# Optimization experiments

Measured on AMD Instinct MI355X. Metric: run time of the kernel, lower is better.

Reference implementation:

```python
import jax, jax.numpy as jnp
import numpy as np

I4_CLIP = 7.0
NUM_HEADS = 16
NUM_KV_HEADS = 4
HEAD_DIM = 64
ROPE_BASE = 10000.0


def fake_quant_i4(w):
    # per-row int4 symmetric fake quantization with straight-through estimator
    row_max = jnp.maximum(jnp.max(jnp.abs(w), axis=-1, keepdims=True), 1e-8)
    scale = row_max / I4_CLIP
    w_deq = jnp.clip(jnp.round(w / scale), -I4_CLIP, I4_CLIP) * scale
    return w + jax.lax.stop_gradient(w_deq - w)


def rms_norm(x):
    eps = jnp.asarray(jnp.finfo(x.dtype).eps, x.dtype)
    return x * jax.lax.rsqrt(jnp.mean(x * x, axis=-1, keepdims=True) + eps)


def rope_cos_sin(seqlen, dtype):
    inv_freq = 1.0 / (ROPE_BASE ** (jnp.arange(0, HEAD_DIM, 2, dtype=jnp.float32) / HEAD_DIM))
    freqs = jnp.outer(jnp.arange(seqlen, dtype=jnp.float32), inv_freq)  # [S, hd/2]
    return jnp.cos(freqs).astype(dtype), jnp.sin(freqs).astype(dtype)


def apply_rotary(x, cos, sin):
    # x: [B, H, S, hd]; cos/sin: [S, hd/2] broadcast over B, H
    half = x.shape[-1] // 2
    x1, x2 = x[..., :half], x[..., half:]
    return jnp.concatenate((x1 * cos + x2 * sin, -x1 * sin + x2 * cos), axis=-1)


def setup_inputs() -> dict:
    key = jax.random.key(0)
    ks = jax.random.split(key, 6)
    dim = NUM_HEADS * HEAD_DIM
    kv_dim = NUM_KV_HEADS * HEAD_DIM
    return {
        "x": jax.random.normal(ks[0], (2, 2048, dim), jnp.float32),
        "w_q": jax.random.normal(ks[1], (dim, dim), jnp.float32) * 0.02,
        "w_k": jax.random.normal(ks[2], (kv_dim, dim), jnp.float32) * 0.02,
        "w_v": jax.random.normal(ks[3], (kv_dim, dim), jnp.float32) * 0.02,
        "w_proj": jax.random.normal(ks[4], (dim, dim), jnp.float32) * 0.02,
        "q_gain": jnp.ones((NUM_HEADS,), jnp.float32),
    }


def reference(x, w_q, w_k, w_v, w_proj, q_gain):
    bsz, seqlen, dim = x.shape
    rep = NUM_HEADS // NUM_KV_HEADS

    wq, wk, wv, wp = (fake_quant_i4(w) for w in (w_q, w_k, w_v, w_proj))

    # projections: F.linear(x, W) = x @ W.T -> [B, S, out]; split heads -> [B, H, S, hd]
    q = (x @ wq.T).reshape(bsz, seqlen, NUM_HEADS, HEAD_DIM).transpose(0, 2, 1, 3)
    k = (x @ wk.T).reshape(bsz, seqlen, NUM_KV_HEADS, HEAD_DIM).transpose(0, 2, 1, 3)
    v = (x @ wv.T).reshape(bsz, seqlen, NUM_KV_HEADS, HEAD_DIM).transpose(0, 2, 1, 3)

    q, k = rms_norm(q), rms_norm(k)
    cos, sin = rope_cos_sin(seqlen, q.dtype)
    q = apply_rotary(q, cos, sin)
    k = apply_rotary(k, cos, sin)
    q = q * q_gain.astype(q.dtype)[None, :, None, None]

    # GQA: expand kv heads
    k = jnp.repeat(k, rep, axis=1)
    v = jnp.repeat(v, rep, axis=1)

    # causal SDPA
    scale = 1.0 / np.sqrt(HEAD_DIM)
    scores = jnp.einsum("bhqd,bhkd->bhqk", q, k) * scale
    causal = jnp.tril(jnp.ones((seqlen, seqlen), dtype=bool))
    scores = jnp.where(causal, scores, jnp.asarray(-jnp.inf, scores.dtype))
    attn = jax.nn.softmax(scores, axis=-1)
    y = jnp.einsum("bhqk,bhkd->bhqd", attn, v)

    y = y.transpose(0, 2, 1, 3).reshape(bsz, seqlen, dim)
    return y @ wp.T
```

## Files before the change

kernel.cpp:

```cpp
#include <hip/hip_runtime.h>


typedef __bf16 bf16x8 __attribute__((ext_vector_type(8)));
typedef __bf16 bf16x4 __attribute__((ext_vector_type(4)));
typedef float  f32x4  __attribute__((ext_vector_type(4)));

__device__ __forceinline__ unsigned short f2bf(float f) {
  __bf16 h = (__bf16)f;
  return __builtin_bit_cast(unsigned short, h);
}

__global__ void quant_rows(const float* __restrict__ src,
                           unsigned short* __restrict__ dst, int ncols) {
  int row = blockIdx.x;
  const float* s = src + (size_t)row * ncols;
  unsigned short* d = dst + (size_t)row * ncols;
  int t = threadIdx.x;
  float v[4]; float mx = 0.f;
#pragma unroll
  for (int i = 0; i < 4; i++) { v[i] = s[t + 256 * i]; mx = fmaxf(mx, fabsf(v[i])); }
#pragma unroll
  for (int m = 1; m < 64; m <<= 1) mx = fmaxf(mx, __shfl_xor(mx, m));
  __shared__ float smx[4];
  if ((t & 63) == 0) smx[t >> 6] = mx;
  __syncthreads();
  mx = fmaxf(fmaxf(smx[0], smx[1]), fmaxf(smx[2], smx[3]));
  mx = fmaxf(mx, 1e-8f);
  float scale = mx / 7.0f;
#pragma unroll
  for (int i = 0; i < 4; i++) {
    float q = rintf(v[i] / scale);
    q = fminf(fmaxf(q, -7.0f), 7.0f);
    d[t + 256 * i] = f2bf(q * scale);
  }
}

__global__ void cvt_bf16(const float* __restrict__ src,
                         unsigned short* __restrict__ dst, int n) {
  int i = (blockIdx.x * 256 + threadIdx.x) * 4;
  if (i >= n) return;
  float4 f = *(const float4*)(src + i);
  ushort4 o;
  o.x = f2bf(f.x); o.y = f2bf(f.y); o.z = f2bf(f.z); o.w = f2bf(f.w);
  *(ushort4*)(dst + i) = o;
}

#define GLDS(g, l)                                                            \
  __builtin_amdgcn_global_load_lds((const __attribute__((address_space(1))) void*)(g), \
                                   (__attribute__((address_space(3))) void*)(l), 16, 0, 0)

__global__ __launch_bounds__(256, 2) void gemm_bt(
    const unsigned short* __restrict__ A, const unsigned short* __restrict__ Bw,
    float* __restrict__ C, int N, int K, int nbn) {
  int bm = blockIdx.x / nbn, bn = blockIdx.x % nbn;
  int tid = threadIdx.x, w = tid >> 6, lane = tid & 63;
  int l15 = lane & 15, lh = lane >> 4;
  __shared__ __align__(16) unsigned short ldsA[2][128 * 64];
  __shared__ __align__(16) unsigned short ldsB[2][128 * 64];
  int wr = w >> 1, wc = w & 1;
  f32x4 zero = {0.f, 0.f, 0.f, 0.f};
  f32x4 acc[4][4];
#pragma unroll
  for (int i = 0; i < 4; i++)
#pragma unroll
    for (int j = 0; j < 4; j++) acc[i][j] = zero;

  int srow = lane >> 3, schunk = (lane & 7) ^ (lane >> 3);
  const unsigned short* gA0 = A  + (size_t)(bm * 128 + srow) * K + schunk * 8;
  const unsigned short* gB0 = Bw + (size_t)(bn * 128 + srow) * K + schunk * 8;

  int nk = K >> 6;
#pragma unroll
  for (int it = 0; it < 4; it++) {
    int seg = w * 4 + it;
    GLDS(gA0 + (size_t)(seg * 8) * K, (unsigned short*)ldsA[0] + seg * 512);
    GLDS(gB0 + (size_t)(seg * 8) * K, (unsigned short*)ldsB[0] + seg * 512);
  }
  __syncthreads();
  int cur = 0;
  for (int kt = 0; kt < nk; kt++) {
    if (kt + 1 < nk) {
      int k0 = (kt + 1) * 64;
#pragma unroll
      for (int it = 0; it < 4; it++) {
        int seg = w * 4 + it;
        GLDS(gA0 + (size_t)(seg * 8) * K + k0, (unsigned short*)ldsA[cur ^ 1] + seg * 512);
        GLDS(gB0 + (size_t)(seg * 8) * K + k0, (unsigned short*)ldsB[cur ^ 1] + seg * 512);
      }
    }
    const unsigned short* cA = ldsA[cur];
    const unsigned short* cB = ldsB[cur];
#pragma unroll
    for (int ks = 0; ks < 2; ks++) {
      bf16x8 af[4], bfr[4];
#pragma unroll
      for (int fm = 0; fm < 4; fm++) {
        int row = wr * 64 + fm * 16 + l15;
        int slot = (ks * 4 + lh) ^ (row & 7);
        af[fm] = *(const bf16x8*)(cA + row * 64 + slot * 8);
      }
#pragma unroll
      for (int fn = 0; fn < 4; fn++) {
        int row = wc * 64 + fn * 16 + l15;
        int slot = (ks * 4 + lh) ^ (row & 7);
        bfr[fn] = *(const bf16x8*)(cB + row * 64 + slot * 8);
      }
#pragma unroll
      for (int fm = 0; fm < 4; fm++)
#pragma unroll
        for (int fn = 0; fn < 4; fn++)
          acc[fm][fn] = __builtin_amdgcn_mfma_f32_16x16x32_bf16(af[fm], bfr[fn], acc[fm][fn], 0, 0, 0);
    }
    __syncthreads();
    cur ^= 1;
  }
#pragma unroll
  for (int fm = 0; fm < 4; fm++) {
    int r0 = bm * 128 + wr * 64 + fm * 16 + lh * 4;
#pragma unroll
    for (int fn = 0; fn < 4; fn++) {
      int c = bn * 128 + wc * 64 + fn * 16 + l15;
#pragma unroll
      for (int reg = 0; reg < 4; reg++)
        C[(size_t)(r0 + reg) * N + c] = acc[fm][fn][reg];
    }
  }
}

__global__ __launch_bounds__(256, 2) void gemm_qkv(
    const unsigned short* __restrict__ A, const unsigned short* __restrict__ Bw,
    const float* __restrict__ gainp,
    unsigned short* __restrict__ qb, unsigned short* __restrict__ kbp,
    unsigned short* __restrict__ vbp) {
  const int K = 1024;
  int bm = blockIdx.x / 12, bn = blockIdx.x % 12;
  int tid = threadIdx.x, w = tid >> 6, lane = tid & 63;
  int l15 = lane & 15, lh = lane >> 4;
  __shared__ __align__(16) unsigned short ldsA[2][128 * 64];
  __shared__ __align__(16) unsigned short ldsB[2][128 * 64];
  int wr = w >> 1, wc = w & 1;
  f32x4 zero = {0.f, 0.f, 0.f, 0.f};
  f32x4 acc[4][4];
#pragma unroll
  for (int i = 0; i < 4; i++)
#pragma unroll
    for (int j = 0; j < 4; j++) acc[i][j] = zero;

  int srow = lane >> 3, schunk = (lane & 7) ^ (lane >> 3);
  const unsigned short* gA0 = A  + (size_t)(bm * 128 + srow) * K + schunk * 8;
  const unsigned short* gB0 = Bw + (size_t)(bn * 128 + srow) * K + schunk * 8;

#pragma unroll
  for (int it = 0; it < 4; it++) {
    int seg = w * 4 + it;
    GLDS(gA0 + (size_t)(seg * 8) * K, (unsigned short*)ldsA[0] + seg * 512);
    GLDS(gB0 + (size_t)(seg * 8) * K, (unsigned short*)ldsB[0] + seg * 512);
  }
  __syncthreads();
  int cur = 0;
  for (int kt = 0; kt < 16; kt++) {
    if (kt + 1 < 16) {
      int k0 = (kt + 1) * 64;
#pragma unroll
      for (int it = 0; it < 4; it++) {
        int seg = w * 4 + it;
        GLDS(gA0 + (size_t)(seg * 8) * K + k0, (unsigned short*)ldsA[cur ^ 1] + seg * 512);
        GLDS(gB0 + (size_t)(seg * 8) * K + k0, (unsigned short*)ldsB[cur ^ 1] + seg * 512);
      }
    }
    const unsigned short* cA = ldsA[cur];
    const unsigned short* cB = ldsB[cur];
#pragma unroll
    for (int ks = 0; ks < 2; ks++) {
      bf16x8 af[4], bfr[4];
#pragma unroll
      for (int fm = 0; fm < 4; fm++) {
        int row = wr * 64 + fm * 16 + l15;
        int slot = (ks * 4 + lh) ^ (row & 7);
        af[fm] = *(const bf16x8*)(cA + row * 64 + slot * 8);
      }
#pragma unroll
      for (int fn = 0; fn < 4; fn++) {
        int row = wc * 64 + fn * 16 + l15;
        int slot = (ks * 4 + lh) ^ (row & 7);
        bfr[fn] = *(const bf16x8*)(cB + row * 64 + slot * 8);
      }
#pragma unroll
      for (int fm = 0; fm < 4; fm++)
#pragma unroll
        for (int fn = 0; fn < 4; fn++)
          acc[fm][fn] = __builtin_amdgcn_mfma_f32_16x16x32_bf16(af[fm], bfr[fn], acc[fm][fn], 0, 0, 0);
    }
    __syncthreads();
    cur ^= 1;
  }

  int hid = bn * 2 + wc;
  int rbase = bm * 128 + wr * 64;
  if (hid >= 20) {
    int vh = hid - 20;
#pragma unroll
    for (int fm = 0; fm < 4; fm++)
#pragma unroll
      for (int reg = 0; reg < 4; reg++) {
        int r = rbase + fm * 16 + lh * 4 + reg;
        int b = r >> 11, s = r & 2047;
        unsigned short* dst = vbp + (((size_t)(b * 4 + vh) * 2048 + s) << 6);
#pragma unroll
        for (int fn = 0; fn < 4; fn++)
          dst[fn * 16 + l15] = f2bf(acc[fm][fn][reg]);
      }
  } else {
    bool isq = hid < 16;
    float gn = isq ? gainp[hid] : 1.0f;
    float invf0 = __expf(-0.28782313662425572f * (float)l15);
    float invf1 = __expf(-0.28782313662425572f * (float)(l15 + 16));
#pragma unroll
    for (int fm = 0; fm < 4; fm++)
#pragma unroll
      for (int reg = 0; reg < 4; reg++) {
        float y0 = acc[fm][0][reg], y1 = acc[fm][1][reg];
        float y2 = acc[fm][2][reg], y3 = acc[fm][3][reg];
        float ss = y0 * y0 + y1 * y1 + y2 * y2 + y3 * y3;
        ss += __shfl_xor(ss, 1); ss += __shfl_xor(ss, 2);
        ss += __shfl_xor(ss, 4); ss += __shfl_xor(ss, 8);
        float rn = rsqrtf(ss * 0.015625f + 1.1920929e-7f);
        y0 *= rn; y1 *= rn; y2 *= rn; y3 *= rn;
        int r = rbase + fm * 16 + lh * 4 + reg;
        int b = r >> 11, s = r & 2047;
        float c0, s0n, c1, s1n;
        __sincosf((float)s * invf0, &s0n, &c0);
        __sincosf((float)s * invf1, &s1n, &c1);
        float o0 = (y0 * c0 + y2 * s0n) * gn;
        float o1 = (y1 * c1 + y3 * s1n) * gn;
        float o2 = (y2 * c0 - y0 * s0n) * gn;
        float o3 = (y3 * c1 - y1 * s1n) * gn;
        unsigned short* dst = isq
          ? qb  + (((size_t)(b * 16 + hid) * 2048 + s) << 6)
          : kbp + (((size_t)(b * 4 + (hid - 16)) * 2048 + s) << 6);
        dst[l15]      = f2bf(o0);
        dst[l15 + 16] = f2bf(o1);
        dst[l15 + 32] = f2bf(o2);
        dst[l15 + 48] = f2bf(o3);
      }
  }
}

__global__ void v_transpose(const unsigned short* __restrict__ vbp,
                            unsigned short* __restrict__ vt) {
  int bid = blockIdx.x;
  int st = bid & 31, bk = bid >> 5;
  __shared__ unsigned short tile[64][72];
  int t = threadIdx.x;
  int sl = t >> 2, d0 = (t & 3) * 16;
  const unsigned short* src = vbp + (((size_t)bk * 2048 + st * 64 + sl) << 6) + d0;
  *(ushort4*)&tile[sl][d0]      = *(const ushort4*)(src);
  *(ushort4*)&tile[sl][d0 + 4]  = *(const ushort4*)(src + 4);
  *(ushort4*)&tile[sl][d0 + 8]  = *(const ushort4*)(src + 8);
  *(ushort4*)&tile[sl][d0 + 12] = *(const ushort4*)(src + 12);
  __syncthreads();
  int d = t >> 2, p0 = (t & 3) * 16;
  unsigned short* dst = vt + ((size_t)bk * 64 + d) * 2048 + st * 64 + p0;
#pragma unroll
  for (int jo = 0; jo < 16; jo += 4) {
    ushort4 a;
#pragma unroll
    for (int j = 0; j < 4; j++) {
      int p = p0 + jo + j;
      int c = ((p & 3) << 4) | (p >> 2);
      ((unsigned short*)&a)[j] = tile[c][d];
    }
    *(ushort4*)(dst + jo) = a;
  }
}

#define PSTR 72

template<bool MASK>
__device__ __forceinline__ void attn_tile(
    int kv0, int q0, int l15, int lh, float M2,
    const unsigned short* ldsK, const unsigned short* ldsV, unsigned short* pw,
    const bf16x8 (&qf)[2][2], float (&lsum)[2][4], f32x4 (&o)[2][4]) {
  const float K2 = 0.18033688011112042f;
  f32x4 zero = {0.f, 0.f, 0.f, 0.f};
  f32x4 sc[2][4];
#pragma unroll
  for (int fm = 0; fm < 2; fm++)
#pragma unroll
    for (int fn = 0; fn < 4; fn++) sc[fm][fn] = zero;
#pragma unroll
  for (int ks = 0; ks < 2; ks++) {
    bf16x8 kf[4];
#pragma unroll
    for (int fn = 0; fn < 4; fn++) {
      int row = fn * 16 + l15;
      int slot = (ks * 4 + lh) ^ (row & 7);
      kf[fn] = *(const bf16x8*)(ldsK + row * 64 + slot * 8);
    }
#pragma unroll
    for (int fm = 0; fm < 2; fm++)
#pragma unroll
      for (int fn = 0; fn < 4; fn++)
        sc[fm][fn] = __builtin_amdgcn_mfma_f32_16x16x32_bf16(qf[fm][ks], kf[fn], sc[fm][fn], 0, 0, 0);
  }
#pragma unroll
  for (int fm = 0; fm < 2; fm++)
#pragma unroll
    for (int r = 0; r < 4; r++) {
      bf16x4 pk;
      float ls = 0.f;
#pragma unroll
      for (int fn = 0; fn < 4; fn++) {
        float s = __builtin_fmaf(sc[fm][fn][r], K2, -M2);
        if (MASK) {
          int col = kv0 + fn * 16 + l15;
          int row = q0 + fm * 16 + lh * 4 + r;
          if (col > row) s = -1e30f;
        }
        float p = __builtin_amdgcn_exp2f(s);
        ls += p;
        pk[fn] = (__bf16)p;
      }
      *(bf16x4*)(pw + (fm * 16 + lh * 4 + r) * PSTR + l15 * 4) = pk;
      lsum[fm][r] += ls;
    }
  asm volatile("s_waitcnt lgkmcnt(0)" ::: "memory");
  __builtin_amdgcn_sched_barrier(0);
#pragma unroll
  for (int ks2 = 0; ks2 < 2; ks2++) {
    bf16x8 vf[4], pf[2];
#pragma unroll
    for (int fn = 0; fn < 4; fn++) {
      int row = fn * 16 + l15;
      int slot = (ks2 * 4 + lh) ^ (row & 7);
      vf[fn] = *(const bf16x8*)(ldsV + row * 64 + slot * 8);
    }
#pragma unroll
    for (int fm = 0; fm < 2; fm++)
      pf[fm] = *(const bf16x8*)(pw + (fm * 16 + l15) * PSTR + ks2 * 32 + lh * 8);
#pragma unroll
    for (int fm = 0; fm < 2; fm++)
#pragma unroll
      for (int fn = 0; fn < 4; fn++)
        o[fm][fn] = __builtin_amdgcn_mfma_f32_16x16x32_bf16(pf[fm], vf[fn], o[fm][fn], 0, 0, 0);
  }
}

__global__ __launch_bounds__(256, 3) void attn_fwd(
    const unsigned short* __restrict__ qbuf, const unsigned short* __restrict__ kb,
    const unsigned short* __restrict__ vtb, const float* __restrict__ gain,
    unsigned short* __restrict__ ob, float* __restrict__ pO,
    float* __restrict__ pL) {
  int bid = blockIdx.x;
  int cid = 39 - (bid >> 5);
  int bh = bid & 31;
  int b = bh >> 4, h = bh & 15;
  int q, ch;
  if (cid < 4)       { q = cid;             ch = 0; }
  else if (cid < 12) { q = (cid + 4) >> 1;  ch = (cid + 4) & 1; }
  else if (cid < 24) { q = (cid + 12) / 3;  ch = (cid + 12) % 3; }
  else               { q = (cid + 24) >> 2; ch = (cid + 24) & 3; }
  int nt = 2 * q + 2;
  int t0 = ch * 8;
  int t1 = (t0 + 8 < nt) ? t0 + 8 : nt;
  bool direct = (cid < 4);

  int tid = threadIdx.x;
  int w = tid >> 6, lane = tid & 63;
  int l15 = lane & 15, lh = lane >> 4;
  int q0 = q * 128 + w * 32;
  int kvh = h >> 2;
  const unsigned short* Q  = qbuf + (size_t)(b * 16 + h) * (2048 * 64);
  const unsigned short* Kg = kb   + (size_t)(b * 4 + kvh) * (2048 * 64);
  const unsigned short* Vg = vtb  + (size_t)(b * 4 + kvh) * (64 * 2048);

  __shared__ __align__(16) unsigned short ldsK[2][64 * 64];
  __shared__ __align__(16) unsigned short ldsV[2][64 * 64];
  __shared__ __align__(16) unsigned short plds[4][32 * PSTR];
  unsigned short* pw = plds[w];

  float gn = gain[h];
  float M2 = __builtin_fmaf(fabsf(gn), 1.46f, 0.02f);

  bf16x8 qf[2][2];
#pragma unroll
  for (int fm = 0; fm < 2; fm++)
#pragma unroll
    for (int ks = 0; ks < 2; ks++)
      qf[fm][ks] = *(const bf16x8*)(Q + (q0 + fm * 16 + l15) * 64 + ks * 32 + lh * 8);

  f32x4 zero = {0.f, 0.f, 0.f, 0.f};
  f32x4 o[2][4];
  float lsum[2][4];
#pragma unroll
  for (int fm = 0; fm < 2; fm++)
#pragma unroll
    for (int r = 0; r < 4; r++) { lsum[fm][r] = 0.f; o[fm][r] = zero; }

  int srow = lane >> 3;
  int schunk = (lane & 7) ^ (lane >> 3);
  int full = q0 >> 6;

#pragma unroll
  for (int it = 0; it < 2; it++) {
    int seg = w * 2 + it;
    GLDS(Kg + (size_t)(t0 * 64 + seg * 8 + srow) * 64 + schunk * 8,
         (unsigned short*)ldsK[0] + seg * 512);
    GLDS(Vg + (size_t)(seg * 8 + srow) * 2048 + t0 * 64 + schunk * 8,
         (unsigned short*)ldsV[0] + seg * 512);
  }
  __syncthreads();
  int cur = 0;
  for (int t = t0; t < t1; t++) {
    int kv0 = t * 64;
    if (t + 1 < t1) {
      int kn = kv0 + 64;
#pragma unroll
      for (int it = 0; it < 2; it++) {
        int seg = w * 2 + it;
        GLDS(Kg + (size_t)(kn + seg * 8 + srow) * 64 + schunk * 8,
             (unsigned short*)ldsK[cur ^ 1] + seg * 512);
        GLDS(Vg + (size_t)(seg * 8 + srow) * 2048 + kn + schunk * 8,
             (unsigned short*)ldsV[cur ^ 1] + seg * 512);
      }
    }
    if (t < full)
      attn_tile<false>(kv0, q0, l15, lh, M2, ldsK[cur], ldsV[cur], pw, qf, lsum, o);
    else if (kv0 <= q0 + 31)
      attn_tile<true>(kv0, q0, l15, lh, M2, ldsK[cur], ldsV[cur], pw, qf, lsum, o);
    __syncthreads();
    cur ^= 1;
  }

  if (direct) {
#pragma unroll
    for (int fm = 0; fm < 2; fm++)
#pragma unroll
      for (int r = 0; r < 4; r++) {
        float l = lsum[fm][r];
        l += __shfl_xor(l, 1); l += __shfl_xor(l, 2);
        l += __shfl_xor(l, 4); l += __shfl_xor(l, 8);
        float inv = 1.0f / l;
        int row = q0 + fm * 16 + lh * 4 + r;
#pragma unroll
        for (int fn = 0; fn < 4; fn++)
          ob[(size_t)(b * 2048 + row) * 1024 + h * 64 + fn * 16 + l15] =
              f2bf(o[fm][fn][r] * inv);
      }
  } else {
    int slot = bh * 36 + (cid - 4);
    float* po = pO + ((size_t)slot << 13);
    float* pl = pL + slot * 128;
#pragma unroll
    for (int fm = 0; fm < 2; fm++)
#pragma unroll
      for (int r = 0; r < 4; r++) {
        float l = lsum[fm][r];
        l += __shfl_xor(l, 1); l += __shfl_xor(l, 2);
        l += __shfl_xor(l, 4); l += __shfl_xor(l, 8);
        int row = w * 32 + fm * 16 + lh * 4 + r;
        if (l15 == 0) pl[row] = l;
#pragma unroll
        for (int fn = 0; fn < 4; fn++)
          po[row * 64 + fn * 16 + l15] = o[fm][fn][r];
      }
  }
}

__global__ __launch_bounds__(256) void attn_finalize(
    const float* __restrict__ pO, const float* __restrict__ pL,
    unsigned short* __restrict__ ob) {
  int bid = blockIdx.x;
  int q = 4 + (bid % 12);
  int bh = bid / 12;
  int b = bh >> 4, h = bh & 15;
  int nc = (2 * q + 9) >> 3;
  int cum = (q < 8) ? 2 * q - 4 : ((q < 12) ? 3 * q - 12 : 4 * q - 24);
  int sbase = bh * 36 + (cum - 4);

  int tid = threadIdx.x;
  int row = tid >> 1, half = tid & 1;
  f32x4 s[8];
#pragma unroll
  for (int j = 0; j < 8; j++) s[j] = (f32x4){0.f, 0.f, 0.f, 0.f};
  float l = 0.f;
  for (int c = 0; c < nc; c++) {
    const float* po = pO + (((size_t)(sbase + c)) << 13) + row * 64 + half * 32;
    l += pL[(sbase + c) * 128 + row];
#pragma unroll
    for (int j = 0; j < 8; j++) s[j] += *(const f32x4*)(po + j * 4);
  }
  float inv = 1.0f / l;
  unsigned short* dst =
      ob + (size_t)(b * 2048 + q * 128 + row) * 1024 + h * 64 + half * 32;
#pragma unroll
  for (int j = 0; j < 8; j++) {
    ushort4 u;
    u.x = f2bf(s[j][0] * inv); u.y = f2bf(s[j][1] * inv);
    u.z = f2bf(s[j][2] * inv); u.w = f2bf(s[j][3] * inv);
    *(ushort4*)(dst + j * 4) = u;
  }
}

extern "C" void kernel_launch(void* const* d_in, const int* in_sizes, int n_in,
                              void* d_out, int out_size, void* d_ws, size_t ws_size,
                              hipStream_t stream) {
  const float* x    = (const float*)d_in[0];
  const float* w_q  = (const float*)d_in[1];
  const float* w_k  = (const float*)d_in[2];
  const float* w_v  = (const float*)d_in[3];
  const float* w_p  = (const float*)d_in[4];
  const float* gain = (const float*)d_in[5];
  float* out = (float*)d_out;

  char* ws = (char*)d_ws;
  unsigned short* x_bf  = (unsigned short*)ws;
  unsigned short* wqkv  = (unsigned short*)(ws + (8u << 20));
  unsigned short* wp    = (unsigned short*)(ws + (11u << 20));
  unsigned short* qbuf  = (unsigned short*)(ws + (13u << 20));
  unsigned short* kbuf  = (unsigned short*)(ws + (21u << 20));
  unsigned short* vbuf  = (unsigned short*)(ws + (23u << 20));
  unsigned short* vtbuf = (unsigned short*)(ws + (25u << 20));
  unsigned short* aout  = (unsigned short*)(ws + (27u << 20));
  float*          pO    = (float*)(ws + (35u << 20));
  float*          pL    = (float*)(ws + (72u << 20));

  quant_rows<<<1024, 256, 0, stream>>>(w_q, wqkv, 1024);
  quant_rows<<<256, 256, 0, stream>>>(w_k, wqkv + 1024 * 1024, 1024);
  quant_rows<<<256, 256, 0, stream>>>(w_v, wqkv + 1280 * 1024, 1024);
  quant_rows<<<1024, 256, 0, stream>>>(w_p, wp, 1024);
  cvt_bf16<<<4096, 256, 0, stream>>>(x, x_bf, 4194304);
  gemm_qkv<<<32 * 12, 256, 0, stream>>>(x_bf, wqkv, gain, qbuf, kbuf, vbuf);
  v_transpose<<<256, 256, 0, stream>>>(vbuf, vtbuf);
  attn_fwd<<<1280, 256, 0, stream>>>(qbuf, kbuf, vtbuf, gain, aout, pO, pL);
  attn_finalize<<<384, 256, 0, stream>>>(pO, pL, aout);
  gemm_bt<<<32 * 8, 256, 0, stream>>>(aout, wp, out, 1024, 1024, 8);
}
```

Before: 114.8 us.

## Double attention query tile per wave, store bf16 partials, fuse weight quant launches

Each attention wave now processes 64 query rows instead of 32, so a block covers 256 queries and each K/V tile loaded into LDS is reused across twice as many rows. Block count halves and occupancy drops to 2 blocks per SM. Split-KV partial outputs are stored as bf16 instead of fp32, and the finalize kernel is reworked to suit. The four weight quantization launches are merged into one kernel. The larger tiles raise register pressure and coarsen the causal-work split, and bf16 partials lose some precision.

Result: no change. 114.9 us (+0.1%).

```diff
diff --git a/kernel.cpp b/kernel.cpp
--- a/kernel.cpp
+++ b/kernel.cpp
@@ -10,11 +10,17 @@
   return __builtin_bit_cast(unsigned short, h);
 }
 
-__global__ void quant_rows(const float* __restrict__ src,
-                           unsigned short* __restrict__ dst, int ncols) {
+__global__ void quant_all(const float* __restrict__ wq, const float* __restrict__ wk,
+                          const float* __restrict__ wv, const float* __restrict__ wp,
+                          unsigned short* __restrict__ wqkv,
+                          unsigned short* __restrict__ wpb) {
   int row = blockIdx.x;
-  const float* s = src + (size_t)row * ncols;
-  unsigned short* d = dst + (size_t)row * ncols;
+  const float* s;
+  unsigned short* d;
+  if (row < 1024)      { s = wq + (size_t)row * 1024;          d = wqkv + (size_t)row * 1024; }
+  else if (row < 1280) { s = wk + (size_t)(row - 1024) * 1024; d = wqkv + (size_t)row * 1024; }
+  else if (row < 1536) { s = wv + (size_t)(row - 1280) * 1024; d = wqkv + (size_t)row * 1024; }
+  else                 { s = wp + (size_t)(row - 1536) * 1024; d = wpb + (size_t)(row - 1536) * 1024; }
   int t = threadIdx.x;
   float v[4]; float mx = 0.f;
 #pragma unroll
@@ -280,12 +286,12 @@
 __device__ __forceinline__ void attn_tile(
     int kv0, int q0, int l15, int lh, float M2,
     const unsigned short* ldsK, const unsigned short* ldsV, unsigned short* pw,
-    const bf16x8 (&qf)[2][2], float (&lsum)[2][4], f32x4 (&o)[2][4]) {
+    const bf16x8 (&qf)[4][2], float (&lsum)[4][4], f32x4 (&o)[4][4]) {
   const float K2 = 0.18033688011112042f;
   f32x4 zero = {0.f, 0.f, 0.f, 0.f};
-  f32x4 sc[2][4];
-#pragma unroll
-  for (int fm = 0; fm < 2; fm++)
+  f32x4 sc[4][4];
+#pragma unroll
+  for (int fm = 0; fm < 4; fm++)
 #pragma unroll
     for (int fn = 0; fn < 4; fn++) sc[fm][fn] = zero;
 #pragma unroll
@@ -298,13 +304,13 @@
       kf[fn] = *(const bf16x8*)(ldsK + row * 64 + slot * 8);
     }
 #pragma unroll
-    for (int fm = 0; fm < 2; fm++)
+    for (int fm = 0; fm < 4; fm++)
 #pragma unroll
       for (int fn = 0; fn < 4; fn++)
         sc[fm][fn] = __builtin_amdgcn_mfma_f32_16x16x32_bf16(qf[fm][ks], kf[fn], sc[fm][fn], 0, 0, 0);
   }
 #pragma unroll
-  for (int fm = 0; fm < 2; fm++)
+  for (int fm = 0; fm < 4; fm++)
 #pragma unroll
     for (int r = 0; r < 4; r++) {
       bf16x4 pk;
@@ -328,7 +334,7 @@
   __builtin_amdgcn_sched_barrier(0);
 #pragma unroll
   for (int ks2 = 0; ks2 < 2; ks2++) {
-    bf16x8 vf[4], pf[2];
+    bf16x8 vf[4], pf[4];
 #pragma unroll
     for (int fn = 0; fn < 4; fn++) {
       int row = fn * 16 + l15;
@@ -336,39 +342,39 @@
       vf[fn] = *(const bf16x8*)(ldsV + row * 64 + slot * 8);
     }
 #pragma unroll
-    for (int fm = 0; fm < 2; fm++)
+    for (int fm = 0; fm < 4; fm++)
       pf[fm] = *(const bf16x8*)(pw + (fm * 16 + l15) * PSTR + ks2 * 32 + lh * 8);
 #pragma unroll
-    for (int fm = 0; fm < 2; fm++)
+    for (int fm = 0; fm < 4; fm++)
 #pragma unroll
       for (int fn = 0; fn < 4; fn++)
         o[fm][fn] = __builtin_amdgcn_mfma_f32_16x16x32_bf16(pf[fm], vf[fn], o[fm][fn], 0, 0, 0);
   }
 }
 
-__global__ __launch_bounds__(256, 3) void attn_fwd(
+__global__ __launch_bounds__(256, 2) void attn_fwd(
     const unsigned short* __restrict__ qbuf, const unsigned short* __restrict__ kb,
     const unsigned short* __restrict__ vtb, const float* __restrict__ gain,
-    unsigned short* __restrict__ ob, float* __restrict__ pO,
+    unsigned short* __restrict__ ob, unsigned short* __restrict__ pO,
     float* __restrict__ pL) {
   int bid = blockIdx.x;
-  int cid = 39 - (bid >> 5);
+  int cid = 19 - (bid >> 5);
   int bh = bid & 31;
   int b = bh >> 4, h = bh & 15;
-  int q, ch;
-  if (cid < 4)       { q = cid;             ch = 0; }
-  else if (cid < 12) { q = (cid + 4) >> 1;  ch = (cid + 4) & 1; }
-  else if (cid < 24) { q = (cid + 12) / 3;  ch = (cid + 12) % 3; }
-  else               { q = (cid + 24) >> 2; ch = (cid + 24) & 3; }
-  int nt = 2 * q + 2;
+  int qb, ch;
+  if (cid < 2)       { qb = cid;                 ch = 0; }
+  else if (cid < 6)  { qb = 2 + ((cid - 2) >> 1); ch = (cid - 2) & 1; }
+  else if (cid < 12) { qb = 4 + (cid - 6) / 3;    ch = (cid - 6) % 3; }
+  else               { qb = 6 + ((cid - 12) >> 2); ch = (cid - 12) & 3; }
+  int nt = 4 * qb + 4;
   int t0 = ch * 8;
   int t1 = (t0 + 8 < nt) ? t0 + 8 : nt;
-  bool direct = (cid < 4);
+  bool direct = (cid < 2);
 
   int tid = threadIdx.x;
   int w = tid >> 6, lane = tid & 63;
   int l15 = lane & 15, lh = lane >> 4;
-  int q0 = q * 128 + w * 32;
+  int q0 = qb * 256 + w * 64;
   int kvh = h >> 2;
   const unsigned short* Q  = qbuf + (size_t)(b * 16 + h) * (2048 * 64);
   const unsigned short* Kg = kb   + (size_t)(b * 4 + kvh) * (2048 * 64);
@@ -376,24 +382,24 @@
 
   __shared__ __align__(16) unsigned short ldsK[2][64 * 64];
   __shared__ __align__(16) unsigned short ldsV[2][64 * 64];
-  __shared__ __align__(16) unsigned short plds[4][32 * PSTR];
+  __shared__ __align__(16) unsigned short plds[4][64 * PSTR];
   unsigned short* pw = plds[w];
 
   float gn = gain[h];
   float M2 = __builtin_fmaf(fabsf(gn), 1.46f, 0.02f);
 
-  bf16x8 qf[2][2];
-#pragma unroll
-  for (int fm = 0; fm < 2; fm++)
+  bf16x8 qf[4][2];
+#pragma unroll
+  for (int fm = 0; fm < 4; fm++)
 #pragma unroll
     for (int ks = 0; ks < 2; ks++)
       qf[fm][ks] = *(const bf16x8*)(Q + (q0 + fm * 16 + l15) * 64 + ks * 32 + lh * 8);
 
   f32x4 zero = {0.f, 0.f, 0.f, 0.f};
-  f32x4 o[2][4];
-  float lsum[2][4];
-#pragma unroll
-  for (int fm = 0; fm < 2; fm++)
+  f32x4 o[4][4];
+  float lsum[4][4];
+#pragma unroll
+  for (int fm = 0; fm < 4; fm++)
 #pragma unroll
     for (int r = 0; r < 4; r++) { lsum[fm][r] = 0.f; o[fm][r] = zero; }
 
@@ -426,7 +432,7 @@
     }
     if (t < full)
       attn_tile<false>(kv0, q0, l15, lh, M2, ldsK[cur], ldsV[cur], pw, qf, lsum, o);
-    else if (kv0 <= q0 + 31)
+    else if (t == full)
       attn_tile<true>(kv0, q0, l15, lh, M2, ldsK[cur], ldsV[cur], pw, qf, lsum, o);
     __syncthreads();
     cur ^= 1;
@@ -434,7 +440,7 @@
 
   if (direct) {
 #pragma unroll
-    for (int fm = 0; fm < 2; fm++)
+    for (int fm = 0; fm < 4; fm++)
 #pragma unroll
       for (int r = 0; r < 4; r++) {
         float l = lsum[fm][r];
@@ -448,58 +454,68 @@
               f2bf(o[fm][fn][r] * inv);
       }
   } else {
-    int slot = bh * 36 + (cid - 4);
-    float* po = pO + ((size_t)slot << 13);
-    float* pl = pL + slot * 128;
-#pragma unroll
-    for (int fm = 0; fm < 2; fm++)
+    int slot = bh * 18 + (cid - 2);
+    unsigned short* po = pO + ((size_t)slot << 14);
+    float* pl = pL + slot * 256;
+#pragma unroll
+    for (int fm = 0; fm < 4; fm++)
 #pragma unroll
       for (int r = 0; r < 4; r++) {
         float l = lsum[fm][r];
         l += __shfl_xor(l, 1); l += __shfl_xor(l, 2);
         l += __shfl_xor(l, 4); l += __shfl_xor(l, 8);
-        int row = w * 32 + fm * 16 + lh * 4 + r;
+        int row = w * 64 + fm * 16 + lh * 4 + r;
         if (l15 == 0) pl[row] = l;
-#pragma unroll
-        for (int fn = 0; fn < 4; fn++)
-          po[row * 64 + fn * 16 + l15] = o[fm][fn][r];
+        bf16x4 pv;
+#pragma unroll
+        for (int fn = 0; fn < 4; fn++) pv[fn] = (__bf16)o[fm][fn][r];
+        *(bf16x4*)(po + row * 64 + l15 * 4) = pv;
       }
   }
 }
 
 __global__ __launch_bounds__(256) void attn_finalize(
-    const float* __restrict__ pO, const float* __restrict__ pL,
+    const unsigned short* __restrict__ pO, const float* __restrict__ pL,
     unsigned short* __restrict__ ob) {
   int bid = blockIdx.x;
-  int q = 4 + (bid % 12);
-  int bh = bid / 12;
+  int qb = 2 + bid % 6;
+  int bh = bid / 6;
   int b = bh >> 4, h = bh & 15;
-  int nc = (2 * q + 9) >> 3;
-  int cum = (q < 8) ? 2 * q - 4 : ((q < 12) ? 3 * q - 12 : 4 * q - 24);
-  int sbase = bh * 36 + (cum - 4);
-
-  int tid = threadIdx.x;
-  int row = tid >> 1, half = tid & 1;
-  f32x4 s[8];
-#pragma unroll
-  for (int j = 0; j < 8; j++) s[j] = (f32x4){0.f, 0.f, 0.f, 0.f};
+  const int ncs[6]   = {2, 2, 3, 3, 4, 4};
+  const int sbase[6] = {0, 2, 4, 7, 10, 14};
+  int nc = ncs[qb - 2];
+  int s0 = bh * 18 + sbase[qb - 2];
+
+  int row = threadIdx.x;
+  float acc[64];
+#pragma unroll
+  for (int j = 0; j < 64; j++) acc[j] = 0.f;
   float l = 0.f;
   for (int c = 0; c < nc; c++) {
-    const float* po = pO + (((size_t)(sbase + c)) << 13) + row * 64 + half * 32;
-    l += pL[(sbase + c) * 128 + row];
-#pragma unroll
-    for (int j = 0; j < 8; j++) s[j] += *(const f32x4*)(po + j * 4);
+    const unsigned short* po = pO + (((size_t)(s0 + c)) << 14) + row * 64;
+    l += pL[(s0 + c) * 256 + row];
+#pragma unroll
+    for (int j = 0; j < 8; j++) {
+      uint4 u = *(const uint4*)(po + j * 8);
+      const unsigned short* us = (const unsigned short*)&u;
+#pragma unroll
+      for (int e = 0; e < 8; e++) {
+        unsigned int bits = (unsigned int)us[e] << 16;
+        acc[j * 8 + e] += __builtin_bit_cast(float, bits);
+      }
+    }
   }
   float inv = 1.0f / l;
-  unsigned short* dst =
-      ob + (size_t)(b * 2048 + q * 128 + row) * 1024 + h * 64 + half * 32;
-#pragma unroll
-  for (int j = 0; j < 8; j++) {
-    ushort4 u;
-    u.x = f2bf(s[j][0] * inv); u.y = f2bf(s[j][1] * inv);
-    u.z = f2bf(s[j][2] * inv); u.w = f2bf(s[j][3] * inv);
-    *(ushort4*)(dst + j * 4) = u;
-  }
+  unsigned short* dst = ob + (size_t)(b * 2048 + qb * 256 + row) * 1024 + h * 64;
+  unsigned short outv[64];
+#pragma unroll
+  for (int c = 0; c < 64; c++) {
+    int pos = (c & 15) * 4 + (c >> 4);
+    outv[c] = f2bf(acc[pos] * inv);
+  }
+#pragma unroll
+  for (int j = 0; j < 8; j++)
+    *(uint4*)(dst + j * 8) = *(const uint4*)(outv + j * 8);
 }
 
 extern "C" void kernel_launch(void* const* d_in, const int* in_sizes, int n_in,
@@ -522,17 +538,14 @@
   unsigned short* vbuf  = (unsigned short*)(ws + (23u << 20));
   unsigned short* vtbuf = (unsigned short*)(ws + (25u << 20));
   unsigned short* aout  = (unsigned short*)(ws + (27u << 20));
-  float*          pO    = (float*)(ws + (35u << 20));
-  float*          pL    = (float*)(ws + (72u << 20));
-
-  quant_rows<<<1024, 256, 0, stream>>>(w_q, wqkv, 1024);
-  quant_rows<<<256, 256, 0, stream>>>(w_k, wqkv + 1024 * 1024, 1024);
-  quant_rows<<<256, 256, 0, stream>>>(w_v, wqkv + 1280 * 1024, 1024);
-  quant_rows<<<1024, 256, 0, stream>>>(w_p, wp, 1024);
+  unsigned short* pO    = (unsigned short*)(ws + (35u << 20));
+  float*          pL    = (float*)(ws + (55u << 20));
+
+  quant_all<<<2560, 256, 0, stream>>>(w_q, w_k, w_v, w_p, wqkv, wp);
   cvt_bf16<<<4096, 256, 0, stream>>>(x, x_bf, 4194304);
   gemm_qkv<<<32 * 12, 256, 0, stream>>>(x_bf, wqkv, gain, qbuf, kbuf, vbuf);
   v_transpose<<<256, 256, 0, stream>>>(vbuf, vtbuf);
-  attn_fwd<<<1280, 256, 0, stream>>>(qbuf, kbuf, vtbuf, gain, aout, pO, pL);
-  attn_finalize<<<384, 256, 0, stream>>>(pO, pL, aout);
+  attn_fwd<<<640, 256, 0, stream>>>(qbuf, kbuf, vtbuf, gain, aout, pO, pL);
+  attn_finalize<<<192, 256, 0, stream>>>(pO, pL, aout);
   gemm_bt<<<32 * 8, 256, 0, stream>>>(aout, wp, out, 1024, 1024, 8);
 }
```
